# Performance work log

Measured on AMD Instinct MI355X. Metric: run time of the kernel, lower is better.

## Reference

```python
import jax, jax.numpy as jnp
import numpy as np

TQ, TV, B, D, UNITS = 256, 1024, 4, 128, 128
NEG_INF = -1e9


def setup_inputs() -> dict:
    key = jax.random.key(0)
    k1, k2, k3, k4, k5, k6 = jax.random.split(key, 6)
    query = jax.random.normal(k1, (TQ, B, D), dtype=jnp.float32)
    value = jax.random.normal(k2, (TV, B, D), dtype=jnp.float32)
    mask = jax.random.randint(k3, (TV, B), 0, 2).astype(bool)
    # guarantee at least one valid key position per batch element
    mask = mask.at[0].set(True)
    # Dense kernels (glorot-uniform-like scaled normals are fine for a reference)
    W1 = jax.random.normal(k4, (D, UNITS), dtype=jnp.float32) * (1.0 / np.sqrt(D))
    W2 = jax.random.normal(k5, (D, UNITS), dtype=jnp.float32) * (1.0 / np.sqrt(D))
    # AdditiveAttention use_scale=True -> learnable scale vector of shape (units,)
    scale = jax.random.normal(k6, (UNITS,), dtype=jnp.float32) * (1.0 / np.sqrt(UNITS))
    return {"query": query, "value": value, "mask": mask, "W1": W1, "W2": W2, "scale": scale}


def reference(query, value, mask, W1, W2, scale):
    # time-major -> batch-major
    q = jnp.transpose(query, (1, 0, 2))   # [B, Tq, D]
    v = jnp.transpose(value, (1, 0, 2))   # [B, Tv, D]
    m = jnp.transpose(mask, (1, 0))       # [B, Tv] bool (value mask)

    wq = jnp.einsum('bqd,du->bqu', q, W1)  # [B, Tq, U]
    wk = jnp.einsum('bvd,du->bvu', v, W2)  # [B, Tv, U]

    # additive score: sum_u scale[u] * tanh(wq[b,q,u] + wk[b,v,u]) -> [B, Tq, Tv]
    scores = jnp.einsum('u,bqvu->bqv', scale, jnp.tanh(wq[:, :, None, :] + wk[:, None, :, :]))

    scores = jnp.where(m[:, None, :], scores, NEG_INF)
    attn = jax.nn.softmax(scores, axis=-1)          # [B, Tq, Tv]
    ctx = jnp.einsum('bqv,bvd->bqd', attn, v)       # [B, Tq, D]

    # batch-major -> time-major
    return jnp.transpose(ctx, (1, 0, 2))            # [Tq, B, D]
```

## Files before the change

kernel.cpp:

```cpp
#include <hip/hip_runtime.h>


#define TQ 256
#define TV 1024
#define BB 4
#define DD 128
#define UU 128
#define NEG_INF -1e9f
#define C2LOG2E 2.8853900817779268f

#define QUAD1(Av, Kv, sv, acc)                                     \
  { float d0 = __builtin_fmaf(Av.x, Kv.x, 1.f);                    \
    float d1 = __builtin_fmaf(Av.y, Kv.y, 1.f);                    \
    float d2 = __builtin_fmaf(Av.z, Kv.z, 1.f);                    \
    float d3 = __builtin_fmaf(Av.w, Kv.w, 1.f);                    \
    float m01 = d0 * d1, m23 = d2 * d3;                            \
    float R = __builtin_amdgcn_rcpf(m01 * m23);                    \
    float q01 = R * m23, q23 = R * m01;                            \
    acc = __builtin_fmaf(sv.x, q01 * d1, acc);                     \
    acc = __builtin_fmaf(sv.y, q01 * d0, acc);                     \
    acc = __builtin_fmaf(sv.z, q23 * d3, acc);                     \
    acc = __builtin_fmaf(sv.w, q23 * d2, acc); }

union SharedA {
  struct { float Wl[DD * UU]; float xs[8][DD]; } pj;
  struct { int wsum[4]; float sred[2]; } cp;
};

__global__ __launch_bounds__(256) void prep_kernel(
    const float* __restrict__ query, const float* __restrict__ value,
    const float* __restrict__ W1, const float* __restrict__ W2,
    const int* __restrict__ mask, const float* __restrict__ scale,
    float* __restrict__ Eq, float* __restrict__ Ek,
    int* __restrict__ valid_idx, int* __restrict__ nvalid,
    float* __restrict__ Ssum)
{
  __shared__ SharedA u;
  const int t = threadIdx.x, lane = t & 63, wid = t >> 6;
  const int bid = blockIdx.x;

  if (bid < BB) {
    const int b = bid;
    int m[4];
#pragma unroll
    for (int k = 0; k < 4; ++k) m[k] = mask[(4 * t + k) * BB + b] ? 1 : 0;
    int cnt = m[0] + m[1] + m[2] + m[3];
    int pre = cnt;
#pragma unroll
    for (int off = 1; off < 64; off <<= 1) {
      int y = __shfl_up(pre, off, 64);
      if (lane >= off) pre += y;
    }
    if (lane == 63) u.cp.wsum[wid] = pre;
    float sv_ = (t < UU) ? scale[t] : 0.f;
#pragma unroll
    for (int off = 32; off > 0; off >>= 1) sv_ += __shfl_xor(sv_, off, 64);
    if (t == 0)  u.cp.sred[0] = sv_;
    if (t == 64) u.cp.sred[1] = sv_;
    __syncthreads();
    int base = 0;
#pragma unroll
    for (int w = 0; w < 4; ++w) if (w < wid) base += u.cp.wsum[w];
    int total = u.cp.wsum[0] + u.cp.wsum[1] + u.cp.wsum[2] + u.cp.wsum[3];
    int idx = base + pre - cnt;
#pragma unroll
    for (int k = 0; k < 4; ++k)
      if (m[k]) valid_idx[b * TV + (idx++)] = 4 * t + k;
    for (int i = t; i < TV; i += 256)
      if (i >= total) valid_idx[b * TV + i] = 0;
    if (t == 0) nvalid[b] = total;
    if (b == 0 && t == 0) Ssum[0] = u.cp.sred[0] + u.cp.sred[1];
  } else {
    const int blk = bid - BB;
    const bool isq = blk < (TQ * BB / 8);
    const float* X = isq ? query : value;
    const float* W = isq ? W1 : W2;
    float* E       = isq ? Eq : Ek;
    const int T    = isq ? TQ : TV;
    const int R0   = (isq ? blk : blk - TQ * BB / 8) * 8;

    const float4* Wg = (const float4*)W;
    float4* Wl4 = (float4*)u.pj.Wl;
#pragma unroll
    for (int k = 0; k < 16; ++k)
      Wl4[k * 256 + t] = Wg[k * 256 + t];
    ((float4*)u.pj.xs)[t] = ((const float4*)(X + (size_t)R0 * DD))[t];
    __syncthreads();

    const int half = t >> 7;
    const int uu_ = t & 127;
    float a[4] = {0.f, 0.f, 0.f, 0.f};
#pragma unroll 4
    for (int d = 0; d < DD; ++d) {
      float wv = u.pj.Wl[d * UU + uu_];
#pragma unroll
      for (int i = 0; i < 4; ++i)
        a[i] += u.pj.xs[half * 4 + i][d] * wv;
    }
#pragma unroll
    for (int i = 0; i < 4; ++i) {
      int rf = R0 + half * 4 + i;
      int b2 = rf & (BB - 1), tt = rf >> 2;
      E[((size_t)b2 * T + tt) * UU + uu_] =
          __builtin_amdgcn_exp2f(a[i] * C2LOG2E);
    }
  }
}

__global__ __launch_bounds__(512, 1) void attn_kernel(
    const float* __restrict__ value,
    const float* __restrict__ Eq,
    const float* __restrict__ Ek,
    const float* __restrict__ scale,
    const float* __restrict__ Ssum,
    const int*   __restrict__ valid_idx,
    const int*   __restrict__ nvalid,
    float* __restrict__ out)
{
  const int bid = blockIdx.x;
  const int b   = bid >> 6;
  const int q0  = (bid & 63) * 4;
  const int t   = threadIdx.x;
  const int lane = t & 63;

  __shared__ float4 kv_lds[128 * 32];
  __shared__ float  s_lds[4][TV];
  __shared__ float4 eq_lds[4 * 32];
  __shared__ int    vidx[TV];
  __shared__ float  redm[4][2], redsum[4][2], inv_s[4];
  __shared__ float  part[4][64][2];

  const int nv  = nvalid[b];
  const int nvt = (nv + 127) >> 7;
  const float S = Ssum[0];

  if (t < 256) ((int4*)vidx)[t] = ((const int4*)(valid_idx + b * TV))[t];
  if (t < 128) eq_lds[t] = ((const float4*)Eq)[((size_t)(b * TQ + q0)) * 32 + t];
  __syncthreads();

  const int q  = t >> 7;
  const int vl = t & 127;
  const int sx = vl & 7;
  const float4* S4 = (const float4*)scale;

  for (int tix = 0; tix < nvt; ++tix) {
    if (tix) __syncthreads();
    {
      const float4* gk = (const float4*)Ek;
#pragma unroll
      for (int k = 0; k < 8; ++k) {
        int i = k * 512 + t;
        int r = i >> 5, c = i & 31;
        kv_lds[r * 32 + (c ^ (r & 7))] =
            gk[((size_t)(b * TV + vidx[tix * 128 + r])) * 32 + c];
      }
    }
    __syncthreads();

    const float4* Ar = eq_lds + q * 32;
    const float4* Kr = kv_lds + vl * 32;
    float acc = 0.f;
#pragma unroll 8
    for (int uu = 0; uu < 32; ++uu) {
      float4 A0 = Ar[uu];
      float4 K0 = Kr[uu ^ sx];
      float4 sv = S4[uu];
      QUAD1(A0, K0, sv, acc)
    }
    s_lds[q][tix * 128 + vl] = __builtin_fmaf(-2.f, acc, S);
  }
  __syncthreads();

  const int wslot = (t >> 6) & 1;
  float mm = NEG_INF;
#pragma unroll
  for (int k = 0; k < 8; ++k) {
    int gv = vl + 128 * k;
    float x = (gv < nv) ? s_lds[q][gv] : NEG_INF;
    mm = fmaxf(mm, x);
  }
#pragma unroll
  for (int off = 32; off > 0; off >>= 1)
    mm = fmaxf(mm, __shfl_xor(mm, off, 64));
  if (lane == 0) redm[q][wslot] = mm;
  __syncthreads();
  mm = fmaxf(redm[q][0], redm[q][1]);

  float ssum = 0.f;
#pragma unroll
  for (int k = 0; k < 8; ++k) {
    int gv = vl + 128 * k;
    float x = (gv < nv) ? s_lds[q][gv] : NEG_INF;
    float p = __expf(x - mm);
    s_lds[q][gv] = p;
    ssum += p;
  }
#pragma unroll
  for (int off = 32; off > 0; off >>= 1)
    ssum += __shfl_xor(ssum, off, 64);
  if (lane == 0) redsum[q][wslot] = ssum;
  __syncthreads();
  if (t < 4) inv_s[t] = 1.f / (redsum[t][0] + redsum[t][1]);

  const int vh = (t >> 6) & 1;
  const int dp = t & 63;
  float ax = 0.f, ay = 0.f;

  for (int tix = 0; tix < nvt; ++tix) {
    __syncthreads();
    {
      const float4* gv4 = (const float4*)value;
#pragma unroll
      for (int k = 0; k < 8; ++k) {
        int i = k * 512 + t;
        int r = i >> 5, c = i & 31;
        kv_lds[r * 32 + c] =
            gv4[((size_t)vidx[tix * 128 + r] * BB + b) * 32 + c];
      }
    }
    __syncthreads();

    const float* Vl = (const float*)kv_lds;
    const int lim = min(128, nv - tix * 128);
    const float* prow = &s_lds[q][tix * 128];
    for (int v = vh; v < lim; v += 2) {
      float p = prow[v];
      float2 vv = *(const float2*)(Vl + v * 128 + 2 * dp);
      ax = __builtin_fmaf(p, vv.x, ax);
      ay = __builtin_fmaf(p, vv.y, ay);
    }
  }

  if (vh) { part[q][dp][0] = ax; part[q][dp][1] = ay; }
  __syncthreads();
  if (!vh) {
    float iv = inv_s[q];
    float2 o = make_float2((ax + part[q][dp][0]) * iv,
                           (ay + part[q][dp][1]) * iv);
    *(float2*)&out[((size_t)(q0 + q) * BB + b) * DD + 2 * dp] = o;
  }
}

extern "C" void kernel_launch(void* const* d_in, const int* in_sizes, int n_in,
                              void* d_out, int out_size, void* d_ws, size_t ws_size,
                              hipStream_t stream) {
  const float* query = (const float*)d_in[0];
  const float* value = (const float*)d_in[1];
  const int*   mask  = (const int*)  d_in[2];
  const float* W1    = (const float*)d_in[3];
  const float* W2    = (const float*)d_in[4];
  const float* scale = (const float*)d_in[5];
  float* out = (float*)d_out;

  float* Eq      = (float*)d_ws;
  float* Ek      = Eq + (size_t)BB * TQ * UU;
  int*   vidx    = (int*)(Ek + (size_t)BB * TV * UU);
  int*   nvalid  = vidx + BB * TV;
  float* Ssum    = (float*)(nvalid + BB);

  prep_kernel<<<BB + (TQ + TV) * BB / 8, 256, 0, stream>>>(
      query, value, W1, W2, mask, scale, Eq, Ek, vidx, nvalid, Ssum);
  attn_kernel<<<BB * TQ / 4, 512, 0, stream>>>(
      value, Eq, Ek, scale, Ssum, vidx, nvalid, out);
}
```

Before: 55.73 us.

## Halve queries per attention block, split score lanes, restructure PV and projection

The attention kernel now handles two queries per block, launching twice as many blocks with relaxed launch bounds. The score loop splits the unit dimension across four lanes with shuffle reductions, and scale and Eq are swizzled into LDS. The PV loop uses unrolled fixed-width chunks with a four-way row split, and the projection reads W directly from global instead of staging it in shared memory. The aim is more parallelism and occupancy, at the cost of reloading the key and value tiles for every pair of queries.

```diff
diff --git a/kernel.cpp b/kernel.cpp
--- a/kernel.cpp
+++ b/kernel.cpp
@@ -22,11 +22,6 @@
     acc = __builtin_fmaf(sv.z, q23 * d3, acc);                     \
     acc = __builtin_fmaf(sv.w, q23 * d2, acc); }
 
-union SharedA {
-  struct { float Wl[DD * UU]; float xs[8][DD]; } pj;
-  struct { int wsum[4]; float sred[2]; } cp;
-};
-
 __global__ __launch_bounds__(256) void prep_kernel(
     const float* __restrict__ query, const float* __restrict__ value,
     const float* __restrict__ W1, const float* __restrict__ W2,
@@ -35,7 +30,8 @@
     int* __restrict__ valid_idx, int* __restrict__ nvalid,
     float* __restrict__ Ssum)
 {
-  __shared__ SharedA u;
+  __shared__ int   wsum[4];
+  __shared__ float sred[2];
   const int t = threadIdx.x, lane = t & 63, wid = t >> 6;
   const int bid = blockIdx.x;
 
@@ -51,17 +47,17 @@
       int y = __shfl_up(pre, off, 64);
       if (lane >= off) pre += y;
     }
-    if (lane == 63) u.cp.wsum[wid] = pre;
+    if (lane == 63) wsum[wid] = pre;
     float sv_ = (t < UU) ? scale[t] : 0.f;
 #pragma unroll
     for (int off = 32; off > 0; off >>= 1) sv_ += __shfl_xor(sv_, off, 64);
-    if (t == 0)  u.cp.sred[0] = sv_;
-    if (t == 64) u.cp.sred[1] = sv_;
+    if (t == 0)  sred[0] = sv_;
+    if (t == 64) sred[1] = sv_;
     __syncthreads();
     int base = 0;
 #pragma unroll
-    for (int w = 0; w < 4; ++w) if (w < wid) base += u.cp.wsum[w];
-    int total = u.cp.wsum[0] + u.cp.wsum[1] + u.cp.wsum[2] + u.cp.wsum[3];
+    for (int w = 0; w < 4; ++w) if (w < wid) base += wsum[w];
+    int total = wsum[0] + wsum[1] + wsum[2] + wsum[3];
     int idx = base + pre - cnt;
 #pragma unroll
     for (int k = 0; k < 4; ++k)
@@ -69,45 +65,39 @@
     for (int i = t; i < TV; i += 256)
       if (i >= total) valid_idx[b * TV + i] = 0;
     if (t == 0) nvalid[b] = total;
-    if (b == 0 && t == 0) Ssum[0] = u.cp.sred[0] + u.cp.sred[1];
+    if (b == 0 && t == 0) Ssum[0] = sred[0] + sred[1];
   } else {
-    const int blk = bid - BB;
-    const bool isq = blk < (TQ * BB / 8);
+    const int R0 = (bid - BB) * 8;
+    const bool isq = (R0 < TQ * BB);
     const float* X = isq ? query : value;
     const float* W = isq ? W1 : W2;
     float* E       = isq ? Eq : Ek;
     const int T    = isq ? TQ : TV;
-    const int R0   = (isq ? blk : blk - TQ * BB / 8) * 8;
-
-    const float4* Wg = (const float4*)W;
-    float4* Wl4 = (float4*)u.pj.Wl;
-#pragma unroll
-    for (int k = 0; k < 16; ++k)
-      Wl4[k * 256 + t] = Wg[k * 256 + t];
-    ((float4*)u.pj.xs)[t] = ((const float4*)(X + (size_t)R0 * DD))[t];
-    __syncthreads();
-
+    const int Rb   = isq ? R0 : (R0 - TQ * BB);
+    const int uu_  = t & 127;
     const int half = t >> 7;
-    const int uu_ = t & 127;
-    float a[4] = {0.f, 0.f, 0.f, 0.f};
-#pragma unroll 4
+    const float* x0 = X + (size_t)(Rb + half * 4) * DD;
+    float a0 = 0.f, a1 = 0.f, a2 = 0.f, a3 = 0.f;
+#pragma unroll 8
     for (int d = 0; d < DD; ++d) {
-      float wv = u.pj.Wl[d * UU + uu_];
-#pragma unroll
-      for (int i = 0; i < 4; ++i)
-        a[i] += u.pj.xs[half * 4 + i][d] * wv;
-    }
+      float wv = W[d * UU + uu_];
+      a0 = __builtin_fmaf(x0[d], wv, a0);
+      a1 = __builtin_fmaf(x0[DD + d], wv, a1);
+      a2 = __builtin_fmaf(x0[2 * DD + d], wv, a2);
+      a3 = __builtin_fmaf(x0[3 * DD + d], wv, a3);
+    }
+    float av[4] = {a0, a1, a2, a3};
 #pragma unroll
     for (int i = 0; i < 4; ++i) {
-      int rf = R0 + half * 4 + i;
+      int rf = Rb + half * 4 + i;
       int b2 = rf & (BB - 1), tt = rf >> 2;
       E[((size_t)b2 * T + tt) * UU + uu_] =
-          __builtin_amdgcn_exp2f(a[i] * C2LOG2E);
+          __builtin_amdgcn_exp2f(av[i] * C2LOG2E);
     }
   }
 }
 
-__global__ __launch_bounds__(512, 1) void attn_kernel(
+__global__ __launch_bounds__(512, 4) void attn_kernel(
     const float* __restrict__ value,
     const float* __restrict__ Eq,
     const float* __restrict__ Ek,
@@ -118,95 +108,116 @@
     float* __restrict__ out)
 {
   const int bid = blockIdx.x;
-  const int b   = bid >> 6;
-  const int q0  = (bid & 63) * 4;
+  const int b   = bid >> 7;
+  const int q0  = (bid & 127) * 2;
   const int t   = threadIdx.x;
   const int lane = t & 63;
 
-  __shared__ float4 kv_lds[128 * 32];
-  __shared__ float  s_lds[4][TV];
-  __shared__ float4 eq_lds[4 * 32];
-  __shared__ int    vidx[TV];
-  __shared__ float  redm[4][2], redsum[4][2], inv_s[4];
-  __shared__ float  part[4][64][2];
+  __shared__ float4 kv[128 * 32];
+  __shared__ float  s_lds[2][TV];
+  __shared__ float4 eq_lds[2 * 32];
+  __shared__ float4 sc_lds[32];
+  __shared__ float  redm[2][4], reds[2][4], inv_s[2];
+  __shared__ float  part[3][2][DD];
 
   const int nv  = nvalid[b];
   const int nvt = (nv + 127) >> 7;
   const float S = Ssum[0];
 
-  if (t < 256) ((int4*)vidx)[t] = ((const int4*)(valid_idx + b * TV))[t];
-  if (t < 128) eq_lds[t] = ((const float4*)Eq)[((size_t)(b * TQ + q0)) * 32 + t];
-  __syncthreads();
-
-  const int q  = t >> 7;
-  const int vl = t & 127;
+  if (t < 64) {
+    int row = t >> 5, c = t & 31;
+    eq_lds[row * 32 + (c ^ (c >> 3))] =
+        ((const float4*)Eq)[((size_t)(b * TQ + q0 + row)) * 32 + c];
+  } else if (t < 96) {
+    int c = t & 31;
+    sc_lds[c ^ (c >> 3)] = ((const float4*)scale)[c];
+  }
+
+  const int vl = t >> 2;
+  const int uq = t & 3;
   const int sx = vl & 7;
-  const float4* S4 = (const float4*)scale;
 
   for (int tix = 0; tix < nvt; ++tix) {
-    if (tix) __syncthreads();
+    int rows[8];
+    const int rb = b * TV + tix * 128 + (t >> 5);
+#pragma unroll
+    for (int k = 0; k < 8; ++k) rows[k] = valid_idx[rb + 16 * k];
+    __syncthreads();
     {
       const float4* gk = (const float4*)Ek;
 #pragma unroll
       for (int k = 0; k < 8; ++k) {
         int i = k * 512 + t;
         int r = i >> 5, c = i & 31;
-        kv_lds[r * 32 + (c ^ (r & 7))] =
-            gk[((size_t)(b * TV + vidx[tix * 128 + r])) * 32 + c];
+        kv[r * 32 + (c ^ (r & 7))] = gk[((size_t)(b * TV + rows[k])) * 32 + c];
       }
     }
     __syncthreads();
 
-    const float4* Ar = eq_lds + q * 32;
-    const float4* Kr = kv_lds + vl * 32;
-    float acc = 0.f;
-#pragma unroll 8
-    for (int uu = 0; uu < 32; ++uu) {
-      float4 A0 = Ar[uu];
-      float4 K0 = Kr[uu ^ sx];
-      float4 sv = S4[uu];
-      QUAD1(A0, K0, sv, acc)
-    }
-    s_lds[q][tix * 128 + vl] = __builtin_fmaf(-2.f, acc, S);
-  }
-  __syncthreads();
-
-  const int wslot = (t >> 6) & 1;
+    float acc0 = 0.f, acc1 = 0.f;
+    const float4* Kr = kv + vl * 32;
+#pragma unroll
+    for (int j = 0; j < 8; ++j) {
+      int uu = uq * 8 + j;
+      float4 K  = Kr[uu ^ sx];
+      int es = uu ^ uq;
+      float4 A0 = eq_lds[es];
+      float4 A1 = eq_lds[32 + es];
+      float4 sv = sc_lds[es];
+      QUAD1(A0, K, sv, acc0)
+      QUAD1(A1, K, sv, acc1)
+    }
+    acc0 += __shfl_xor(acc0, 1, 64); acc0 += __shfl_xor(acc0, 2, 64);
+    acc1 += __shfl_xor(acc1, 1, 64); acc1 += __shfl_xor(acc1, 2, 64);
+    if (uq == 0) {
+      s_lds[0][tix * 128 + vl] = __builtin_fmaf(-2.f, acc0, S);
+      s_lds[1][tix * 128 + vl] = __builtin_fmaf(-2.f, acc1, S);
+    }
+  }
+  __syncthreads();
+
+  const int sq = t >> 8;
+  const int si = t & 255;
+  const int ws = (t >> 6) & 3;
+  float xv[4];
   float mm = NEG_INF;
 #pragma unroll
-  for (int k = 0; k < 8; ++k) {
-    int gv = vl + 128 * k;
-    float x = (gv < nv) ? s_lds[q][gv] : NEG_INF;
-    mm = fmaxf(mm, x);
+  for (int k = 0; k < 4; ++k) {
+    int gv = si + 256 * k;
+    xv[k] = (gv < nv) ? s_lds[sq][gv] : NEG_INF;
+    mm = fmaxf(mm, xv[k]);
   }
 #pragma unroll
   for (int off = 32; off > 0; off >>= 1)
     mm = fmaxf(mm, __shfl_xor(mm, off, 64));
-  if (lane == 0) redm[q][wslot] = mm;
-  __syncthreads();
-  mm = fmaxf(redm[q][0], redm[q][1]);
+  if (lane == 0) redm[sq][ws] = mm;
+  __syncthreads();
+  mm = fmaxf(fmaxf(redm[sq][0], redm[sq][1]), fmaxf(redm[sq][2], redm[sq][3]));
 
   float ssum = 0.f;
 #pragma unroll
-  for (int k = 0; k < 8; ++k) {
-    int gv = vl + 128 * k;
-    float x = (gv < nv) ? s_lds[q][gv] : NEG_INF;
-    float p = __expf(x - mm);
-    s_lds[q][gv] = p;
+  for (int k = 0; k < 4; ++k) {
+    float p = __expf(xv[k] - mm);
+    s_lds[sq][si + 256 * k] = p;
     ssum += p;
   }
 #pragma unroll
   for (int off = 32; off > 0; off >>= 1)
     ssum += __shfl_xor(ssum, off, 64);
-  if (lane == 0) redsum[q][wslot] = ssum;
-  __syncthreads();
-  if (t < 4) inv_s[t] = 1.f / (redsum[t][0] + redsum[t][1]);
-
-  const int vh = (t >> 6) & 1;
-  const int dp = t & 63;
-  float ax = 0.f, ay = 0.f;
+  if (lane == 0) reds[sq][ws] = ssum;
+  __syncthreads();
+  if (t < 2)
+    inv_s[t] = 1.f / (reds[t][0] + reds[t][1] + reds[t][2] + reds[t][3]);
+
+  const int vq = t >> 7;
+  const int dp = t & 127;
+  float a0 = 0.f, a1 = 0.f;
 
   for (int tix = 0; tix < nvt; ++tix) {
+    int rows[8];
+    const int rb = b * TV + tix * 128 + (t >> 5);
+#pragma unroll
+    for (int k = 0; k < 8; ++k) rows[k] = valid_idx[rb + 16 * k];
     __syncthreads();
     {
       const float4* gv4 = (const float4*)value;
@@ -214,30 +225,34 @@
       for (int k = 0; k < 8; ++k) {
         int i = k * 512 + t;
         int r = i >> 5, c = i & 31;
-        kv_lds[r * 32 + c] =
-            gv4[((size_t)vidx[tix * 128 + r] * BB + b) * 32 + c];
+        kv[r * 32 + c] = gv4[((size_t)rows[k] * BB + b) * 32 + c];
       }
     }
     __syncthreads();
 
-    const float* Vl = (const float*)kv_lds;
-    const int lim = min(128, nv - tix * 128);
-    const float* prow = &s_lds[q][tix * 128];
-    for (int v = vh; v < lim; v += 2) {
-      float p = prow[v];
-      float2 vv = *(const float2*)(Vl + v * 128 + 2 * dp);
-      ax = __builtin_fmaf(p, vv.x, ax);
-      ay = __builtin_fmaf(p, vv.y, ay);
-    }
-  }
-
-  if (vh) { part[q][dp][0] = ax; part[q][dp][1] = ay; }
-  __syncthreads();
-  if (!vh) {
-    float iv = inv_s[q];
-    float2 o = make_float2((ax + part[q][dp][0]) * iv,
-                           (ay + part[q][dp][1]) * iv);
-    *(float2*)&out[((size_t)(q0 + q) * BB + b) * DD + 2 * dp] = o;
+    const float* Vf = (const float*)kv;
+    const float4* p40 = (const float4*)&s_lds[0][tix * 128 + vq * 32];
+    const float4* p41 = (const float4*)&s_lds[1][tix * 128 + vq * 32];
+#pragma unroll
+    for (int c8 = 0; c8 < 8; ++c8) {
+      float4 p0 = p40[c8];
+      float4 p1 = p41[c8];
+      const float* Vr = Vf + (vq * 32 + c8 * 4) * 128 + dp;
+      float v0 = Vr[0], v1 = Vr[128], v2 = Vr[256], v3 = Vr[384];
+      a0 = __builtin_fmaf(p0.x, v0, a0); a1 = __builtin_fmaf(p1.x, v0, a1);
+      a0 = __builtin_fmaf(p0.y, v1, a0); a1 = __builtin_fmaf(p1.y, v1, a1);
+      a0 = __builtin_fmaf(p0.z, v2, a0); a1 = __builtin_fmaf(p1.z, v2, a1);
+      a0 = __builtin_fmaf(p0.w, v3, a0); a1 = __builtin_fmaf(p1.w, v3, a1);
+    }
+  }
+
+  if (vq) { part[vq - 1][0][dp] = a0; part[vq - 1][1][dp] = a1; }
+  __syncthreads();
+  if (vq == 0) {
+    float o0 = a0 + part[0][0][dp] + part[1][0][dp] + part[2][0][dp];
+    float o1 = a1 + part[0][1][dp] + part[1][1][dp] + part[2][1][dp];
+    out[((size_t)q0 * BB + b) * DD + dp]       = o0 * inv_s[0];
+    out[((size_t)(q0 + 1) * BB + b) * DD + dp] = o1 * inv_s[1];
   }
 }
 
@@ -260,6 +275,6 @@
 
   prep_kernel<<<BB + (TQ + TV) * BB / 8, 256, 0, stream>>>(
       query, value, W1, W2, mask, scale, Eq, Ek, vidx, nvalid, Ssum);
-  attn_kernel<<<BB * TQ / 4, 512, 0, stream>>>(
+  attn_kernel<<<BB * TQ / 2, 512, 0, stream>>>(
       value, Eq, Ek, scale, Ssum, vidx, nvalid, out);
 }
```

After: 51.03 us. -8.4%, faster.
